# Kernel optimization log

Measured on AMD Instinct MI355X. Metric: run time of the kernel, lower is better.

The kernel has to match this reference:

```python
import jax, jax.numpy as jnp
import numpy as np

B, P, N, E = 32, 1024, 1024, 128
HQ = 128  # head_num * qkv_dim == embedding_dim
SQRT_E = 11.313708498984761
LOGIT_CLIP = 10.0


def setup_inputs() -> dict:
    key = jax.random.key(0)
    ks = jax.random.split(key, 16)
    s = 1.0 / np.sqrt(E)
    return {
        "encoded_nodes": jax.random.normal(ks[0], (B, N, E), jnp.float32),
        "encoded_q1": jax.random.normal(ks[1], (B, P, E), jnp.float32),
        "encoded_q2": jax.random.normal(ks[2], (B, P, E), jnp.float32),
        "encoded_last_node": jax.random.normal(ks[3], (B, P, E), jnp.float32),
        "load": jax.random.uniform(ks[4], (B, P), jnp.float32),
        "left": jax.random.uniform(ks[5], (B, P), jnp.float32),
        "cur_dist": jax.random.uniform(ks[6], (B, P, N), jnp.float32),
        "log_scale": jnp.ones((), jnp.float32),
        "ninf_mask": jnp.zeros((B, P, N), jnp.float32),
        "Wq1": jax.random.normal(ks[7], (E, HQ), jnp.float32) * s,
        "Wq2": jax.random.normal(ks[8], (E, HQ), jnp.float32) * s,
        "Wq_last": jax.random.normal(ks[9], (E + 2, HQ), jnp.float32) * s,
        "Wk": jax.random.normal(ks[10], (E, HQ), jnp.float32) * s,
        "Wv": jax.random.normal(ks[11], (E, HQ), jnp.float32) * s,
        "AFT_dist_alpha": jnp.ones((1,), jnp.float32),
        "probs_dist_alpha": jnp.ones((1,), jnp.float32),
    }


def reference(encoded_nodes, encoded_q1, encoded_q2, encoded_last_node, load, left,
              cur_dist, log_scale, ninf_mask, Wq1, Wq2, Wq_last, Wk, Wv,
              AFT_dist_alpha, probs_dist_alpha):
    # set_kv / set_q1 / set_q2
    k = encoded_nodes @ Wk                      # [B,N,HQ]
    v = encoded_nodes @ Wv                      # [B,N,HQ]
    single_head_key = jnp.swapaxes(encoded_nodes, 1, 2)  # [B,E,N]
    q1 = encoded_q1 @ Wq1                       # [B,P,HQ]
    q2 = encoded_q2 @ Wq2

    input_cat = jnp.concatenate([encoded_last_node, load[:, :, None], left[:, :, None]], axis=2)
    q_last = input_cat @ Wq_last                # [B,P,HQ]
    q = q1 + q2 + q_last

    cur_dist_out = -cur_dist                    # [B,P,N]
    sigmoid_q = jax.nn.sigmoid(q)
    bias_scale = log_scale * AFT_dist_alpha[0] * cur_dist_out + ninf_mask
    e_bias = jnp.exp(bias_scale)                # [B,P,N]
    ek = jnp.exp(k)                             # [B,N,HQ]
    num = jnp.nan_to_num(jnp.einsum('bpn,bnd->bpd', e_bias, ek * v))
    den = jnp.nan_to_num(jnp.einsum('bpn,bnd->bpd', e_bias, ek)) + 1e-20
    AFT_out = sigmoid_q * (num / den)           # [B,P,HQ]

    score = jnp.einsum('bpd,bdn->bpn', AFT_out, single_head_key)
    score_scaled = score / SQRT_E + log_scale * probs_dist_alpha[0] * cur_dist_out
    score_clipped = LOGIT_CLIP * jnp.tanh(score_scaled)
    probs = jax.nn.softmax(score_clipped + ninf_mask, axis=2)
    return probs
```

## Files before the change

### kernel.cpp

```cpp
#include <hip/hip_runtime.h>
#include <math.h>

#define Bb 32
#define Pp 1024
#define Nn 1024

typedef unsigned short u16;
typedef __bf16 bf16x8 __attribute__((ext_vector_type(8)));
typedef float f32x4 __attribute__((ext_vector_type(4)));
typedef u16 us8 __attribute__((ext_vector_type(8)));
typedef u16 us4 __attribute__((ext_vector_type(4)));

#define MFMA __builtin_amdgcn_mfma_f32_16x16x32_bf16

static constexpr float INV_SQRT_E = 0.08838834764831845f;

__device__ __forceinline__ bf16x8 asbf(us8 v) { return __builtin_bit_cast(bf16x8, v); }

__device__ __forceinline__ void bsplit(float x, u16& h, u16& l) {
  unsigned u = __float_as_uint(x);
  unsigned r = u + 0x7FFF + ((u >> 16) & 1);
  h = (u16)(r >> 16);
  float hf = __uint_as_float((unsigned)h << 16);
  float lof = x - hf;
  unsigned u2 = __float_as_uint(lof);
  unsigned r2 = u2 + 0x7FFF + ((u2 >> 16) & 1);
  l = (u16)(r2 >> 16);
}

__device__ __forceinline__ void tsplit(float x, u16& h, u16& l) {
  unsigned u = __float_as_uint(x);
  h = (u16)(u >> 16);
  float lof = x - __uint_as_float(u & 0xFFFF0000u);
  l = (u16)(__float_as_uint(lof) >> 16);
}

__device__ __forceinline__ float exp10tanh(float s) {
  float ax = fabsf(s);
  float u = __expf(-2.0f * ax);
  float r = __builtin_amdgcn_rcpf(1.0f + u);
  float tt = fmaf(-2.0f * u, r, 1.0f);
  tt = copysignf(tt, s);
  return __expf(10.0f * tt);
}

__global__ __launch_bounds__(256) void prep_weights(
    const float* __restrict__ Wq1, const float* __restrict__ Wq2,
    const float* __restrict__ Wql, const float* __restrict__ Wk,
    const float* __restrict__ Wv, u16* __restrict__ wcat_hi, u16* __restrict__ wcat_lo,
    u16* __restrict__ wkv_hi, u16* __restrict__ wkv_lo) {
  int t = threadIdx.x;
  if (blockIdx.x == 0) {
    for (int i = t; i < 128 * 384; i += 256) {
      int c = i / 384, k = i % 384;
      float v = (k < 128) ? Wq1[k * 128 + c]
                          : (k < 256) ? Wq2[(k - 128) * 128 + c] : Wql[(k - 256) * 128 + c];
      u16 h, l;
      bsplit(v, h, l);
      wcat_hi[i] = h;
      wcat_lo[i] = l;
    }
  } else {
    for (int i = t; i < 256 * 128; i += 256) {
      int c = i >> 7, k = i & 127;
      float v = (c < 128) ? Wk[k * 128 + c] : Wv[k * 128 + (c - 128)];
      u16 h, l;
      bsplit(v, h, l);
      wkv_hi[i] = h;
      wkv_lo[i] = l;
    }
  }
}

__global__ __launch_bounds__(256, 1) void kv_prep(
    const float* __restrict__ nodes, const u16* __restrict__ wkv_hi,
    const u16* __restrict__ wkv_lo, u16* __restrict__ ekkP_hi, u16* __restrict__ ekkP_lo,
    u16* __restrict__ nodesP_hi, u16* __restrict__ nodesP_lo) {
  __shared__ u16 a_hi[32 * 136], a_lo[32 * 136];
  __shared__ float kvbuf[32 * 264];
  const int t = threadIdx.x;
  const int xcd = blockIdx.x & 7, jj = blockIdx.x >> 3;
  const int b = xcd * 4 + (jj >> 5);
  const int n0 = (jj & 31) * 32;
  for (int i = t; i < 4096; i += 256) {
    int n = i >> 7, d = i & 127;
    float v = nodes[((long)(b * 1024 + n0 + n)) * 128 + d];
    u16 h, l;
    bsplit(v, h, l);
    a_hi[n * 136 + d] = h;
    a_lo[n * 136 + d] = l;
  }
  __syncthreads();
  const int lane = t & 63, w = t >> 6;
  const int lr = lane & 15, lg = lane >> 4;
  f32x4 acc0[2][4] = {}, acc1[2][4] = {};
#pragma unroll
  for (int ks = 0; ks < 4; ++ks) {
    us8 ah[2], al[2];
#pragma unroll
    for (int mt = 0; mt < 2; ++mt) {
      int ro = (lr + 16 * mt) * 136 + ks * 32 + lg * 8;
      ah[mt] = *(const us8*)&a_hi[ro];
      al[mt] = *(const us8*)&a_lo[ro];
    }
    us8 bh[4], bl[4];
#pragma unroll
    for (int cc = 0; cc < 4; ++cc) {
      long off = (long)((w * 4 + cc) * 16 + lr) * 128 + ks * 32 + lg * 8;
      bh[cc] = *(const us8*)&wkv_hi[off];
      bl[cc] = *(const us8*)&wkv_lo[off];
    }
#pragma unroll
    for (int mt = 0; mt < 2; ++mt)
#pragma unroll
      for (int cc = 0; cc < 4; ++cc) {
        acc0[mt][cc] = MFMA(asbf(ah[mt]), asbf(bh[cc]), acc0[mt][cc], 0, 0, 0);
        acc1[mt][cc] = MFMA(asbf(al[mt]), asbf(bh[cc]), acc1[mt][cc], 0, 0, 0);
        acc1[mt][cc] = MFMA(asbf(ah[mt]), asbf(bl[cc]), acc1[mt][cc], 0, 0, 0);
      }
  }
#pragma unroll
  for (int mt = 0; mt < 2; ++mt)
#pragma unroll
    for (int cc = 0; cc < 4; ++cc) {
      int c = (w * 4 + cc) * 16 + lr;
#pragma unroll
      for (int r = 0; r < 4; ++r)
        kvbuf[(lg * 4 + r + 16 * mt) * 264 + c] = acc0[mt][cc][r] + acc1[mt][cc][r];
    }
  __syncthreads();
#pragma unroll
  for (int jo = 0; jo < 4; ++jo) {
    int c = jo * 64 + (t & 63);
    int i4 = t >> 6;
    int kcol = (c < 128) ? c : (c - 128);
    us8 h8, l8;
#pragma unroll
    for (int jq = 0; jq < 8; ++jq) {
      int n = i4 * 8 + jq;
      float kv = kvbuf[n * 264 + kcol];
      float ek = __expf(kv);
      float val = (c < 128) ? ek * kvbuf[n * 264 + c + 128] : ek;
      u16 h, l;
      bsplit(val, h, l);
      h8[jq] = h;
      l8[jq] = l;
    }
    long o = (((long)b * 128 + (n0 >> 3) + i4) * 256 + c) * 8;
    *(us8*)&ekkP_hi[o] = h8;
    *(us8*)&ekkP_lo[o] = l8;
  }
  {
    int pl = t >> 7, r = t & 127;
    int dgrp = r >> 3, nb = r & 7;
    const u16* src = pl ? a_lo : a_hi;
    u16* dst = pl ? nodesP_lo : nodesP_hi;
#pragma unroll
    for (int i = 0; i < 4; ++i) {
      int n = nb + 8 * i;
      us8 v = *(const us8*)&src[n * 136 + dgrp * 8];
      *(us8*)&dst[(((long)(b * 16 + dgrp)) * 1024 + n0 + n) * 8] = v;
    }
  }
}

__global__ __launch_bounds__(256) void qsig_prep(
    const float* __restrict__ q1m, const float* __restrict__ q2m,
    const float* __restrict__ lnm, const float* __restrict__ loadv,
    const float* __restrict__ leftv, const float* __restrict__ Wql,
    const u16* __restrict__ wcat_hi, const u16* __restrict__ wcat_lo,
    float* __restrict__ qsig) {
  const int t = threadIdx.x;
  const int lane = t & 63, w = t >> 6;
  const int lr = lane & 15, lg = lane >> 4;
  const long p0 = (long)blockIdx.x * 16;
  const long arow = p0 + lr;
  f32x4 qacc[2] = {};
#pragma unroll 2
  for (int s = 0; s < 12; ++s) {
    const float* __restrict__ src = (s < 4) ? q1m : (s < 8) ? q2m : lnm;
    long ao = arow * 128 + (s & 3) * 32 + lg * 8;
    float4 a0 = *(const float4*)&src[ao];
    float4 a1 = *(const float4*)&src[ao + 4];
    float av[8] = {a0.x, a0.y, a0.z, a0.w, a1.x, a1.y, a1.z, a1.w};
    us8 ah, al;
#pragma unroll
    for (int jq = 0; jq < 8; ++jq) {
      u16 hh, ll;
      tsplit(av[jq], hh, ll);
      ah[jq] = hh;
      al[jq] = ll;
    }
#pragma unroll
    for (int cf = 0; cf < 2; ++cf) {
      int c = w * 32 + cf * 16 + lr;
      us8 bh = *(const us8*)&wcat_hi[c * 384 + s * 32 + lg * 8];
      us8 bl = *(const us8*)&wcat_lo[c * 384 + s * 32 + lg * 8];
      qacc[cf] = MFMA(asbf(ah), asbf(bh), qacc[cf], 0, 0, 0);
      qacc[cf] = MFMA(asbf(al), asbf(bh), qacc[cf], 0, 0, 0);
      qacc[cf] = MFMA(asbf(ah), asbf(bl), qacc[cf], 0, 0, 0);
    }
  }
#pragma unroll
  for (int cf = 0; cf < 2; ++cf) {
    int c = w * 32 + cf * 16 + lr;
    float wl1 = Wql[128 * 128 + c], wl2 = Wql[129 * 128 + c];
#pragma unroll
    for (int r = 0; r < 4; ++r) {
      int row = lg * 4 + r;
      float qv = qacc[cf][r] + loadv[p0 + row] * wl1 + leftv[p0 + row] * wl2;
      qsig[(p0 + row) * 128 + c] = 1.0f / (1.0f + __expf(-qv));
    }
  }
}

__global__ __launch_bounds__(512, 2) void ndaft_gemm(
    const float* __restrict__ cdist, const float* __restrict__ ninf,
    const u16* __restrict__ ekkP_hi, const u16* __restrict__ ekkP_lo,
    const float* __restrict__ qsig, u16* __restrict__ aftP_hi,
    u16* __restrict__ aftP_lo, u16* __restrict__ bias16,
    const float* __restrict__ logs, const float* __restrict__ aal,
    const float* __restrict__ pal) {
  __shared__ u16 lds[25088];
  const int t = threadIdx.x;
  const int lane = t & 63, w = t >> 6;
  const int lr = lane & 15, lg = lane >> 4;
  const int wr = w >> 2, wc = w & 3;
  const int xcd = blockIdx.x & 7, j = blockIdx.x >> 3;
  const int b = xcd * 4 + (j & 3);
  const int pt = j >> 2;
  const long bp = (long)b * Pp + pt * 128;
  const float c1 = logs[0] * aal[0];
  const float c2 = logs[0] * pal[0];

  const int srow = t >> 2, soct = t & 3;
  const long arow = bp + srow;
  const long tbase = (arow >> 4) * 32768;
  const int spr = srow & 15, sptile = srow >> 4;
  const long bsrc = (long)b * 128 * 2048;

  float4 d0, d1, f0, f1;
  us8 bst[4];
  auto load_regs = [&](int s) {
    long ao = arow * 1024 + s * 32 + soct * 8;
    d0 = *(const float4*)&cdist[ao];
    d1 = *(const float4*)&cdist[ao + 4];
    f0 = *(const float4*)&ninf[ao];
    f1 = *(const float4*)&ninf[ao + 4];
    long sb = bsrc + (long)s * 8192;
#pragma unroll
    for (int i = 0; i < 2; ++i) {
      bst[i] = *(const us8*)&ekkP_hi[sb + (i * 512 + t) * 8];
      bst[i + 2] = *(const us8*)&ekkP_lo[sb + (i * 512 + t) * 8];
    }
  };

  us8 ebh, ebl;
  auto compute_eb = [&](int s) {
    float dv[8] = {d0.x, d0.y, d0.z, d0.w, d1.x, d1.y, d1.z, d1.w};
    float nv[8] = {f0.x, f0.y, f0.z, f0.w, f1.x, f1.y, f1.z, f1.w};
    us8 q8;
#pragma unroll
    for (int jq = 0; jq < 8; ++jq) {
      float e = __expf(fmaf(-c1, dv[jq], nv[jq]));
      u16 h, l;
      tsplit(e, h, l);
      ebh[jq] = h;
      ebl[jq] = l;
      float x = fminf(fmaxf(c2 * dv[jq], 0.f), 15.999f);
      q8[jq] = (nv[jq] < -1e5f) ? (u16)0xFFFF : (u16)(x * 4096.f + 0.5f);
    }
    *(us8*)&bias16[tbase + ((s * 4 + soct) * 16 + spr) * 8] = q8;
  };

  auto write_lds = [&]() {
    *(us8*)&lds[((sptile * 2 + 0) * 4 + soct) * 136 + spr * 8] = ebh;
    *(us8*)&lds[((sptile * 2 + 1) * 4 + soct) * 136 + spr * 8] = ebl;
#pragma unroll
    for (int i = 0; i < 2; ++i) {
      *(us8*)&lds[8704 + (i * 512 + t) * 8] = bst[i];
      *(us8*)&lds[8704 + 8192 + (i * 512 + t) * 8] = bst[i + 2];
    }
  };

  f32x4 acc[4][4] = {};
  load_regs(0);
  for (int s = 0; s < 32; ++s) {
    compute_eb(s);
    __syncthreads();
    write_lds();
    __syncthreads();
    if (s < 31) load_regs(s + 1);
    us8 ah[4], al[4];
#pragma unroll
    for (int mt = 0; mt < 4; ++mt) {
      int ptl = wr * 4 + mt;
      ah[mt] = *(const us8*)&lds[((ptl * 2 + 0) * 4 + lg) * 136 + lr * 8];
      al[mt] = *(const us8*)&lds[((ptl * 2 + 1) * 4 + lg) * 136 + lr * 8];
    }
#pragma unroll
    for (int ct = 0; ct < 4; ++ct) {
      int c = (ct < 2) ? (wc * 32 + ct * 16 + lr) : (96 + wc * 32 + ct * 16 + lr);
      us8 bh = *(const us8*)&lds[8704 + lg * 2048 + c * 8];
      us8 bl = *(const us8*)&lds[8704 + 8192 + lg * 2048 + c * 8];
#pragma unroll
      for (int mt = 0; mt < 4; ++mt) {
        acc[mt][ct] = MFMA(asbf(ah[mt]), asbf(bh), acc[mt][ct], 0, 0, 0);
        acc[mt][ct] = MFMA(asbf(al[mt]), asbf(bh), acc[mt][ct], 0, 0, 0);
        acc[mt][ct] = MFMA(asbf(ah[mt]), asbf(bl), acc[mt][ct], 0, 0, 0);
      }
    }
  }
#pragma unroll
  for (int mt = 0; mt < 4; ++mt)
#pragma unroll
    for (int ct = 0; ct < 2; ++ct) {
      int cn = wc * 32 + ct * 16 + lr;
      int nc = cn >> 3, jq = cn & 7;
#pragma unroll
      for (int r = 0; r < 4; ++r) {
        long gr = bp + wr * 64 + mt * 16 + lg * 4 + r;
        float sig = qsig[gr * 128 + cn];
        float aftv = sig * acc[mt][ct][r] * __builtin_amdgcn_rcpf(acc[mt][ct + 2][r] + 1e-20f);
        u16 h, l;
        bsplit(aftv, h, l);
        long idx = (gr >> 4) * 2048 + (nc * 16 + (gr & 15)) * 8 + jq;
        aftP_hi[idx] = h;
        aftP_lo[idx] = l;
      }
    }
}

__global__ __launch_bounds__(256, 4) void score_softmax(
    const u16* bias16, const u16* __restrict__ aftP_hi, const u16* __restrict__ aftP_lo,
    const u16* __restrict__ nodesP_hi, const u16* __restrict__ nodesP_lo,
    float* out) {
  __shared__ float psum[16 * 4];
  __shared__ float invb[16];
  const int t = threadIdx.x;
  const int lane = t & 63, w = t >> 6;
  const int lr = lane & 15, lg = lane >> 4;
  const int xcd = blockIdx.x & 7, j = blockIdx.x >> 3;
  const int b = xcd * 4 + (j >> 6);
  const int tl = j & 63;
  const int p0 = tl * 16;
  const long bp = (long)b * Pp + p0;
  const int tile = b * 64 + tl;

  f32x4 sacc[16] = {};
#pragma unroll
  for (int ks = 0; ks < 4; ++ks) {
    long aoff = (long)tile * 2048 + ((long)((ks * 4 + lg) * 16 + lr)) * 8;
    us8 ah = *(const us8*)&aftP_hi[aoff];
    us8 al = *(const us8*)&aftP_lo[aoff];
    long nb = ((long)(b * 16 + ks * 4 + lg)) * 1024;
    auto bld = [&](int cf, us8& bh, us8& bl) {
      long o = (nb + w * 256 + cf * 16 + lr) * 8;
      bh = *(const us8*)&nodesP_hi[o];
      bl = *(const us8*)&nodesP_lo[o];
    };
    us8 bh0, bl0, bh1, bl1;
    bld(0, bh0, bl0);
    bld(1, bh1, bl1);
#pragma unroll
    for (int cf = 0; cf < 16; ++cf) {
      us8 nh = bh1, nl = bl1;
      if (cf < 14) bld(cf + 2, nh, nl);
      sacc[cf] = MFMA(asbf(bh0), asbf(ah), sacc[cf], 0, 0, 0);
      sacc[cf] = MFMA(asbf(bl0), asbf(ah), sacc[cf], 0, 0, 0);
      sacc[cf] = MFMA(asbf(bh0), asbf(al), sacc[cf], 0, 0, 0);
      bh0 = bh1; bl0 = bl1; bh1 = nh; bl1 = nl;
    }
  }

  const long btile = (long)tile * 32768;
  float rs = 0.f;
#pragma unroll
  for (int cf = 0; cf < 16; ++cf) {
    int nc = w * 32 + cf * 2 + (lg >> 1);
    int j0 = (lg & 1) * 4;
    us4 q4 = *(const us4*)&bias16[btile + (nc * 16 + lr) * 8 + j0];
#pragma unroll
    for (int r = 0; r < 4; ++r) {
      u16 qv = q4[r];
      float sv = fmaf(sacc[cf][r], INV_SQRT_E, (float)qv * -2.44140625e-4f);
      float e = exp10tanh(sv);
      e = (qv == (u16)0xFFFF) ? 0.f : e;
      sacc[cf][r] = e;
      rs += e;
    }
  }
  rs += __shfl_xor(rs, 16);
  rs += __shfl_xor(rs, 32);
  if (lane < 16) psum[lr * 4 + w] = rs;
  __syncthreads();
  if (t < 16)
    invb[t] = 1.0f / (psum[t * 4] + psum[t * 4 + 1] + psum[t * 4 + 2] + psum[t * 4 + 3]);
  __syncthreads();

  const float inv = invb[lr];
  const long ro = (bp + lr) * (long)Nn + w * 256;
#pragma unroll
  for (int cf = 0; cf < 16; ++cf) {
    float4 v;
    v.x = sacc[cf][0] * inv;
    v.y = sacc[cf][1] * inv;
    v.z = sacc[cf][2] * inv;
    v.w = sacc[cf][3] * inv;
    *(float4*)&out[ro + cf * 16 + lg * 4] = v;
  }
}

extern "C" void kernel_launch(void* const* d_in, const int* in_sizes, int n_in,
                              void* d_out, int out_size, void* d_ws, size_t ws_size,
                              hipStream_t stream) {
  const float* nodes = (const float*)d_in[0];
  const float* q1m = (const float*)d_in[1];
  const float* q2m = (const float*)d_in[2];
  const float* lnm = (const float*)d_in[3];
  const float* loadv = (const float*)d_in[4];
  const float* leftv = (const float*)d_in[5];
  const float* cdist = (const float*)d_in[6];
  const float* logs = (const float*)d_in[7];
  const float* ninf = (const float*)d_in[8];
  const float* Wq1 = (const float*)d_in[9];
  const float* Wq2 = (const float*)d_in[10];
  const float* Wql = (const float*)d_in[11];
  const float* Wk = (const float*)d_in[12];
  const float* Wv = (const float*)d_in[13];
  const float* aalpha = (const float*)d_in[14];
  const float* palpha = (const float*)d_in[15];

  char* ws = (char*)d_ws;
  u16* ekkP_hi = (u16*)ws;
  u16* ekkP_lo = (u16*)(ws + (16ul << 20));
  u16* nodesP_hi = (u16*)(ws + (32ul << 20));
  u16* nodesP_lo = (u16*)(ws + (40ul << 20));
  float* qsig = (float*)(ws + (48ul << 20));
  u16* aftP_hi = (u16*)(ws + (64ul << 20));
  u16* aftP_lo = (u16*)(ws + (72ul << 20));
  u16* wcat_hi = (u16*)(ws + (80ul << 20));
  u16* wcat_lo = wcat_hi + 128 * 384;
  u16* wkv_hi = wcat_lo + 128 * 384;
  u16* wkv_lo = wkv_hi + 256 * 128;
  u16* bias16 = (u16*)d_out;

  prep_weights<<<2, 256, 0, stream>>>(Wq1, Wq2, Wql, Wk, Wv, wcat_hi, wcat_lo, wkv_hi, wkv_lo);
  kv_prep<<<Bb * Nn / 32, 256, 0, stream>>>(nodes, wkv_hi, wkv_lo, ekkP_hi, ekkP_lo,
                                            nodesP_hi, nodesP_lo);
  qsig_prep<<<2048, 256, 0, stream>>>(q1m, q2m, lnm, loadv, leftv, Wql, wcat_hi, wcat_lo,
                                      qsig);
  ndaft_gemm<<<256, 512, 0, stream>>>(cdist, ninf, ekkP_hi, ekkP_lo, qsig, aftP_hi,
                                      aftP_lo, bias16, logs, aalpha, palpha);
  score_softmax<<<Bb * Pp / 16, 256, 0, stream>>>(
      bias16, aftP_hi, aftP_lo, nodesP_hi, nodesP_lo, (float*)d_out);
}
```

Baseline: 363.5 us.

## Double-buffer distance/mask loads and overlap next-stage bias compute with MFMA

The cur_dist/ninf register loads become double-buffered two stages ahead. The exp/split computation of the next stage's bias tile is moved after the LDS write so it overlaps with the current stage's MFMA work. The __syncthreads calls are replaced by an lgkmcnt wait plus a raw s_barrier, so outstanding global loads no longer have to drain at each barrier. In exchange it holds an extra set of 16 floats in registers under a 512-thread, 2-block launch bound, which risks register spills or lower occupancy.

```diff
diff --git a/kernel.cpp b/kernel.cpp
--- a/kernel.cpp
+++ b/kernel.cpp
@@ -214,6 +214,10 @@
   }
 }
 
+struct DFset {
+  float4 d0, d1, f0, f1;
+};
+
 __global__ __launch_bounds__(512, 2) void ndaft_gemm(
     const float* __restrict__ cdist, const float* __restrict__ ninf,
     const u16* __restrict__ ekkP_hi, const u16* __restrict__ ekkP_lo,
@@ -239,14 +243,18 @@
   const int spr = srow & 15, sptile = srow >> 4;
   const long bsrc = (long)b * 128 * 2048;
 
-  float4 d0, d1, f0, f1;
+  DFset dfA, dfB;
   us8 bst[4];
-  auto load_regs = [&](int s) {
+  us8 ebh, ebl;
+
+  auto load_df = [&](DFset& df, int s) {
     long ao = arow * 1024 + s * 32 + soct * 8;
-    d0 = *(const float4*)&cdist[ao];
-    d1 = *(const float4*)&cdist[ao + 4];
-    f0 = *(const float4*)&ninf[ao];
-    f1 = *(const float4*)&ninf[ao + 4];
+    df.d0 = *(const float4*)&cdist[ao];
+    df.d1 = *(const float4*)&cdist[ao + 4];
+    df.f0 = *(const float4*)&ninf[ao];
+    df.f1 = *(const float4*)&ninf[ao + 4];
+  };
+  auto load_bst = [&](int s) {
     long sb = bsrc + (long)s * 8192;
 #pragma unroll
     for (int i = 0; i < 2; ++i) {
@@ -254,11 +262,9 @@
       bst[i + 2] = *(const us8*)&ekkP_lo[sb + (i * 512 + t) * 8];
     }
   };
-
-  us8 ebh, ebl;
-  auto compute_eb = [&](int s) {
-    float dv[8] = {d0.x, d0.y, d0.z, d0.w, d1.x, d1.y, d1.z, d1.w};
-    float nv[8] = {f0.x, f0.y, f0.z, f0.w, f1.x, f1.y, f1.z, f1.w};
+  auto compute_eb = [&](DFset& df, int s) {
+    float dv[8] = {df.d0.x, df.d0.y, df.d0.z, df.d0.w, df.d1.x, df.d1.y, df.d1.z, df.d1.w};
+    float nv[8] = {df.f0.x, df.f0.y, df.f0.z, df.f0.w, df.f1.x, df.f1.y, df.f1.z, df.f1.w};
     us8 q8;
 #pragma unroll
     for (int jq = 0; jq < 8; ++jq) {
@@ -272,7 +278,6 @@
     }
     *(us8*)&bias16[tbase + ((s * 4 + soct) * 16 + spr) * 8] = q8;
   };
-
   auto write_lds = [&]() {
     *(us8*)&lds[((sptile * 2 + 0) * 4 + soct) * 136 + spr * 8] = ebh;
     *(us8*)&lds[((sptile * 2 + 1) * 4 + soct) * 136 + spr * 8] = ebl;
@@ -284,13 +289,23 @@
   };
 
   f32x4 acc[4][4] = {};
-  load_regs(0);
-  for (int s = 0; s < 32; ++s) {
-    compute_eb(s);
-    __syncthreads();
+
+  load_df(dfA, 0);
+  load_df(dfB, 1);
+  load_bst(0);
+  compute_eb(dfA, 0);
+
+  auto stage = [&](int s, DFset& refill, DFset& consume) {
+    asm volatile("s_waitcnt lgkmcnt(0)" ::: "memory");
+    __builtin_amdgcn_s_barrier();
+    __builtin_amdgcn_sched_barrier(0);
     write_lds();
-    __syncthreads();
-    if (s < 31) load_regs(s + 1);
+    asm volatile("s_waitcnt lgkmcnt(0)" ::: "memory");
+    __builtin_amdgcn_s_barrier();
+    __builtin_amdgcn_sched_barrier(0);
+    if (s < 31) load_bst(s + 1);
+    if (s < 30) load_df(refill, s + 2);
+    if (s < 31) compute_eb(consume, s + 1);
     us8 ah[4], al[4];
 #pragma unroll
     for (int mt = 0; mt < 4; ++mt) {
@@ -310,7 +325,14 @@
         acc[mt][ct] = MFMA(asbf(ah[mt]), asbf(bl), acc[mt][ct], 0, 0, 0);
       }
     }
-  }
+  };
+
+#pragma unroll 1
+  for (int s2 = 0; s2 < 32; s2 += 2) {
+    stage(s2, dfA, dfB);
+    stage(s2 + 1, dfB, dfA);
+  }
+
 #pragma unroll
   for (int mt = 0; mt < 4; ++mt)
 #pragma unroll
```

Result: faster. 349.3 us, median of 2 (-3.9%).

## Drop LDS staging in AFT GEMM; each wave computes its own A operand from registers

Applied to the files above, without the earlier changes.

Rewrites ndaft_gemm to run 512 blocks of 256 threads over 64-row tiles without shared memory or barriers. Each wave loads cdist/ninf straight into registers in MFMA A-fragment layout, computes exp-bias splits locally, and reads the B (exp(k), exp(k)*v) fragments directly from global memory with one step of register prefetch. This removes the two __syncthreads per K-step and the LDS round trip. In exchange, all four waves redundantly recompute the same exp and split work and reload the same cdist/ninf rows, which adds VALU and global/L2 traffic.

```diff
diff --git a/kernel.cpp b/kernel.cpp
--- a/kernel.cpp
+++ b/kernel.cpp
@@ -214,114 +214,108 @@
   }
 }
 
-__global__ __launch_bounds__(512, 2) void ndaft_gemm(
+__global__ __launch_bounds__(256, 2) void ndaft_gemm(
     const float* __restrict__ cdist, const float* __restrict__ ninf,
     const u16* __restrict__ ekkP_hi, const u16* __restrict__ ekkP_lo,
     const float* __restrict__ qsig, u16* __restrict__ aftP_hi,
     u16* __restrict__ aftP_lo, u16* __restrict__ bias16,
     const float* __restrict__ logs, const float* __restrict__ aal,
     const float* __restrict__ pal) {
-  __shared__ u16 lds[25088];
   const int t = threadIdx.x;
   const int lane = t & 63, w = t >> 6;
   const int lr = lane & 15, lg = lane >> 4;
-  const int wr = w >> 2, wc = w & 3;
   const int xcd = blockIdx.x & 7, j = blockIdx.x >> 3;
   const int b = xcd * 4 + (j & 3);
   const int pt = j >> 2;
-  const long bp = (long)b * Pp + pt * 128;
+  const long bp = (long)b * Pp + pt * 64;
   const float c1 = logs[0] * aal[0];
   const float c2 = logs[0] * pal[0];
-
-  const int srow = t >> 2, soct = t & 3;
-  const long arow = bp + srow;
-  const long tbase = (arow >> 4) * 32768;
-  const int spr = srow & 15, sptile = srow >> 4;
   const long bsrc = (long)b * 128 * 2048;
-
-  float4 d0, d1, f0, f1;
-  us8 bst[4];
-  auto load_regs = [&](int s) {
-    long ao = arow * 1024 + s * 32 + soct * 8;
-    d0 = *(const float4*)&cdist[ao];
-    d1 = *(const float4*)&cdist[ao + 4];
-    f0 = *(const float4*)&ninf[ao];
-    f1 = *(const float4*)&ninf[ao + 4];
-    long sb = bsrc + (long)s * 8192;
-#pragma unroll
-    for (int i = 0; i < 2; ++i) {
-      bst[i] = *(const us8*)&ekkP_hi[sb + (i * 512 + t) * 8];
-      bst[i + 2] = *(const us8*)&ekkP_lo[sb + (i * 512 + t) * 8];
-    }
-  };
-
-  us8 ebh, ebl;
-  auto compute_eb = [&](int s) {
-    float dv[8] = {d0.x, d0.y, d0.z, d0.w, d1.x, d1.y, d1.z, d1.w};
-    float nv[8] = {f0.x, f0.y, f0.z, f0.w, f1.x, f1.y, f1.z, f1.w};
-    us8 q8;
-#pragma unroll
-    for (int jq = 0; jq < 8; ++jq) {
-      float e = __expf(fmaf(-c1, dv[jq], nv[jq]));
-      u16 h, l;
-      tsplit(e, h, l);
-      ebh[jq] = h;
-      ebl[jq] = l;
-      float x = fminf(fmaxf(c2 * dv[jq], 0.f), 15.999f);
-      q8[jq] = (nv[jq] < -1e5f) ? (u16)0xFFFF : (u16)(x * 4096.f + 0.5f);
-    }
-    *(us8*)&bias16[tbase + ((s * 4 + soct) * 16 + spr) * 8] = q8;
-  };
-
-  auto write_lds = [&]() {
-    *(us8*)&lds[((sptile * 2 + 0) * 4 + soct) * 136 + spr * 8] = ebh;
-    *(us8*)&lds[((sptile * 2 + 1) * 4 + soct) * 136 + spr * 8] = ebl;
-#pragma unroll
-    for (int i = 0; i < 2; ++i) {
-      *(us8*)&lds[8704 + (i * 512 + t) * 8] = bst[i];
-      *(us8*)&lds[8704 + 8192 + (i * 512 + t) * 8] = bst[i + 2];
-    }
-  };
+  const long tile0 = bp >> 4;
+
+  int ccol[4];
+#pragma unroll
+  for (int ct = 0; ct < 4; ++ct)
+    ccol[ct] = ((ct < 2) ? (w * 32 + ct * 16) : (96 + w * 32 + ct * 16)) + lr;
+
+  float4 dc0[4], dc1[4], dn0[4], dn1[4];
+#pragma unroll
+  for (int rg = 0; rg < 4; ++rg) {
+    long ao = (bp + rg * 16 + lr) * 1024 + lg * 8;
+    dc0[rg] = *(const float4*)&cdist[ao];
+    dc1[rg] = *(const float4*)&cdist[ao + 4];
+    dn0[rg] = *(const float4*)&ninf[ao];
+    dn1[rg] = *(const float4*)&ninf[ao + 4];
+  }
+
+  us8 Bh[4], Bl[4];
+  {
+    long sb = bsrc + (long)lg * 2048;
+#pragma unroll
+    for (int ct = 0; ct < 4; ++ct) {
+      Bh[ct] = *(const us8*)&ekkP_hi[sb + ccol[ct] * 8];
+      Bl[ct] = *(const us8*)&ekkP_lo[sb + ccol[ct] * 8];
+    }
+  }
 
   f32x4 acc[4][4] = {};
-  load_regs(0);
+
+#pragma unroll 1
   for (int s = 0; s < 32; ++s) {
-    compute_eb(s);
-    __syncthreads();
-    write_lds();
-    __syncthreads();
-    if (s < 31) load_regs(s + 1);
-    us8 ah[4], al[4];
-#pragma unroll
-    for (int mt = 0; mt < 4; ++mt) {
-      int ptl = wr * 4 + mt;
-      ah[mt] = *(const us8*)&lds[((ptl * 2 + 0) * 4 + lg) * 136 + lr * 8];
-      al[mt] = *(const us8*)&lds[((ptl * 2 + 1) * 4 + lg) * 136 + lr * 8];
-    }
-#pragma unroll
-    for (int ct = 0; ct < 4; ++ct) {
-      int c = (ct < 2) ? (wc * 32 + ct * 16 + lr) : (96 + wc * 32 + ct * 16 + lr);
-      us8 bh = *(const us8*)&lds[8704 + lg * 2048 + c * 8];
-      us8 bl = *(const us8*)&lds[8704 + 8192 + lg * 2048 + c * 8];
-#pragma unroll
-      for (int mt = 0; mt < 4; ++mt) {
-        acc[mt][ct] = MFMA(asbf(ah[mt]), asbf(bh), acc[mt][ct], 0, 0, 0);
-        acc[mt][ct] = MFMA(asbf(al[mt]), asbf(bh), acc[mt][ct], 0, 0, 0);
-        acc[mt][ct] = MFMA(asbf(ah[mt]), asbf(bl), acc[mt][ct], 0, 0, 0);
-      }
-    }
-  }
-#pragma unroll
-  for (int mt = 0; mt < 4; ++mt)
+#pragma unroll
+    for (int rg = 0; rg < 4; ++rg) {
+      float dv[8] = {dc0[rg].x, dc0[rg].y, dc0[rg].z, dc0[rg].w,
+                     dc1[rg].x, dc1[rg].y, dc1[rg].z, dc1[rg].w};
+      float nv[8] = {dn0[rg].x, dn0[rg].y, dn0[rg].z, dn0[rg].w,
+                     dn1[rg].x, dn1[rg].y, dn1[rg].z, dn1[rg].w};
+      us8 ah, al, q8;
+#pragma unroll
+      for (int jq = 0; jq < 8; ++jq) {
+        float e = __expf(fmaf(-c1, dv[jq], nv[jq]));
+        u16 h, l;
+        tsplit(e, h, l);
+        ah[jq] = h;
+        al[jq] = l;
+        float x = fminf(fmaxf(c2 * dv[jq], 0.f), 15.999f);
+        q8[jq] = (nv[jq] < -1e5f) ? (u16)0xFFFF : (u16)(x * 4096.f + 0.5f);
+      }
+      if (w == 0)
+        *(us8*)&bias16[(tile0 + rg) * 32768 + ((s * 4 + lg) * 16 + lr) * 8] = q8;
+      if (s < 31) {
+        long ao = (bp + rg * 16 + lr) * 1024 + (s + 1) * 32 + lg * 8;
+        dc0[rg] = *(const float4*)&cdist[ao];
+        dc1[rg] = *(const float4*)&cdist[ao + 4];
+        dn0[rg] = *(const float4*)&ninf[ao];
+        dn1[rg] = *(const float4*)&ninf[ao + 4];
+      }
+#pragma unroll
+      for (int ct = 0; ct < 4; ++ct) {
+        acc[rg][ct] = MFMA(asbf(ah), asbf(Bh[ct]), acc[rg][ct], 0, 0, 0);
+        acc[rg][ct] = MFMA(asbf(al), asbf(Bh[ct]), acc[rg][ct], 0, 0, 0);
+        acc[rg][ct] = MFMA(asbf(ah), asbf(Bl[ct]), acc[rg][ct], 0, 0, 0);
+      }
+    }
+    if (s < 31) {
+      long sb = bsrc + (long)(s + 1) * 8192 + (long)lg * 2048;
+#pragma unroll
+      for (int ct = 0; ct < 4; ++ct) {
+        Bh[ct] = *(const us8*)&ekkP_hi[sb + ccol[ct] * 8];
+        Bl[ct] = *(const us8*)&ekkP_lo[sb + ccol[ct] * 8];
+      }
+    }
+  }
+
+#pragma unroll
+  for (int rg = 0; rg < 4; ++rg)
 #pragma unroll
     for (int ct = 0; ct < 2; ++ct) {
-      int cn = wc * 32 + ct * 16 + lr;
+      int cn = w * 32 + ct * 16 + lr;
       int nc = cn >> 3, jq = cn & 7;
 #pragma unroll
       for (int r = 0; r < 4; ++r) {
-        long gr = bp + wr * 64 + mt * 16 + lg * 4 + r;
+        long gr = bp + rg * 16 + lg * 4 + r;
         float sig = qsig[gr * 128 + cn];
-        float aftv = sig * acc[mt][ct][r] * __builtin_amdgcn_rcpf(acc[mt][ct + 2][r] + 1e-20f);
+        float aftv = sig * acc[rg][ct][r] * __builtin_amdgcn_rcpf(acc[rg][ct + 2][r] + 1e-20f);
         u16 h, l;
         bsplit(aftv, h, l);
         long idx = (gr >> 4) * 2048 + (nc * 16 + (gr & 15)) * 8 + jq;
@@ -450,7 +444,7 @@
                                             nodesP_hi, nodesP_lo);
   qsig_prep<<<2048, 256, 0, stream>>>(q1m, q2m, lnm, loadv, leftv, Wql, wcat_hi, wcat_lo,
                                       qsig);
-  ndaft_gemm<<<256, 512, 0, stream>>>(cdist, ninf, ekkP_hi, ekkP_lo, qsig, aftP_hi,
+  ndaft_gemm<<<512, 256, 0, stream>>>(cdist, ninf, ekkP_hi, ekkP_lo, qsig, aftP_hi,
                                       aftP_lo, bias16, logs, aalpha, palpha);
   score_softmax<<<Bb * Pp / 16, 256, 0, stream>>>(
       bias16, aftP_hi, aftP_lo, nodesP_hi, nodesP_lo, (float*)d_out);
```

New measurement: 418.4 us. 1.15x slower.
